# Optimization experiments

Measured on AMD Instinct MI355X. Metric: run time of the kernel, lower is better.

## Reference

```python
import jax, jax.numpy as jnp
import numpy as np

B, C, L, D = 8, 16, 512, 256  # batch, channels (attended axis), seq len, d_model


def setup_inputs() -> dict:
    key = jax.random.key(0)
    ks = jax.random.split(key, 9)
    d = D
    x = jax.random.normal(ks[0], (B, C, L, D), dtype=jnp.float32)
    # qkv projection: Linear(d, 3d), xavier_normal weight, zero-ish bias
    Wqkv = jax.random.normal(ks[1], (3 * d, d), dtype=jnp.float32) * (2.0 / (4 * d)) ** 0.5
    bqkv = jnp.zeros((3 * d,), dtype=jnp.float32)
    # additive-attention scorer V: Linear(d, 1)
    Vw = jax.random.normal(ks[2], (1, d), dtype=jnp.float32) * (1.0 / d) ** 0.5
    Vb = jnp.zeros((1,), dtype=jnp.float32)
    bh = jnp.zeros((d,), dtype=jnp.float32)  # nn.Parameter(torch.zeros(d_model))
    ba = jnp.zeros((1,), dtype=jnp.float32)  # nn.Parameter(torch.zeros(1))
    # output projection Linear(d, d)
    Wout = jax.random.normal(ks[3], (d, d), dtype=jnp.float32) * (1.0 / d) ** 0.5
    bout = jnp.zeros((d,), dtype=jnp.float32)
    return {"x": x, "Wqkv": Wqkv, "bqkv": bqkv, "Vw": Vw, "Vb": Vb,
            "bh": bh, "ba": ba, "Wout": Wout, "bout": bout}


def reference(x, Wqkv, bqkv, Vw, Vb, bh, ba, Wout, bout):
    b, c, l, d = x.shape
    # (b, c, l, d) -> (b*l, c, d): attention over the channel axis c per position
    xf = jnp.transpose(x, (0, 2, 1, 3)).reshape(b * l, c, d)
    qkv = xf @ Wqkv.T + bqkv                       # (B, c, 3d)
    q, k, v = jnp.split(qkv, 3, axis=-1)           # each (B, c, d)
    # additive (Bahdanau) score: V(tanh(q_i + k_j + bh)) + ba
    h = jnp.tanh(q[:, :, None, :] + k[:, None, :, :] + bh)  # (B, c, c, d)
    score = jnp.einsum('bqkd,d->bqk', h, Vw[0]) + Vb[0] + ba[0]  # (B, c, c)
    A = jax.nn.softmax(score, axis=-1)             # stable softmax (matches exp(s-max)/sum)
    # torch einsum 'b c c, b c d -> b c d': repeated index -> DIAGONAL of A scales v
    z = jnp.einsum('bcc,bcd->bcd', A, v)           # (B, c, d)
    z = z.reshape(b, l, c, d).transpose(0, 2, 1, 3)  # (b, c, l, d)
    return z @ Wout.T + bout
```

## Files before the change

kernel.cpp:

```cpp
#include <hip/hip_runtime.h>


typedef __attribute__((ext_vector_type(8))) short bf16x8;
typedef __attribute__((ext_vector_type(4))) float f32x4;
typedef __attribute__((ext_vector_type(8))) _Float16 h16x8;
typedef __attribute__((ext_vector_type(4))) _Float16 h16x4;
typedef const __attribute__((address_space(1))) void* gp1_t;
typedef __attribute__((address_space(3))) void* lp3_t;

__device__ __forceinline__ unsigned short f2bf(float f) {
  union { float f; unsigned int u; } v; v.f = f;
  return (unsigned short)((v.u + 0x7FFFu + ((v.u >> 16) & 1u)) >> 16);
}

__device__ __forceinline__ unsigned int cvt_pk_bf16(float a, float b) {
  unsigned int r;
  asm("v_cvt_pk_bf16_f32 %0, %1, %2" : "=v"(r) : "v"(a), "v"(b));
  return r;
}

__global__ __launch_bounds__(256) void ca_prep_kernel(
    const float* __restrict__ Wqkv, const float* __restrict__ Wout,
    const float* __restrict__ bqkv, const float* __restrict__ bh,
    unsigned short* __restrict__ Wqb_t, unsigned short* __restrict__ Wcb_t,
    float* __restrict__ bcomb, float* __restrict__ bsc) {
  const int blk = blockIdx.x;
  if (blk < 64) {
    const int t = blk * 256 + threadIdx.x;
    const int k8 = t >> 9, n = t & 511;
    const float* src = Wqkv + (size_t)n * 256 + k8 * 8;
    const float4 v0 = *(const float4*)src;
    const float4 v1 = *(const float4*)(src + 4);
    bf16x8 o;
    o[0] = (short)f2bf(v0.x); o[1] = (short)f2bf(v0.y);
    o[2] = (short)f2bf(v0.z); o[3] = (short)f2bf(v0.w);
    o[4] = (short)f2bf(v1.x); o[5] = (short)f2bf(v1.y);
    o[6] = (short)f2bf(v1.z); o[7] = (short)f2bf(v1.w);
    *(bf16x8*)(Wqb_t + (size_t)t * 8) = o;
    return;
  }
  const int dp = blk - 64;
  const int e = threadIdx.x;
  if (dp < 2) {
    const int n = dp * 256 + e;
    const float b = bqkv[n] + (n < 256 ? bh[n] : 0.f);
    bsc[n] = b * 1.4426950408889634f;
  }
  const float* wrow = Wout + (size_t)dp * 256;
  float acc = 0.f;
  for (int f = 0; f < 256; ++f)
    acc = fmaf(wrow[f], Wqkv[(size_t)(512 + f) * 256 + e], acc);
  Wcb_t[((size_t)(e >> 3) * 256 + dp) * 8 + (e & 7)] = f2bf(acc);
  if (e == 0) {
    float b = 0.f;
    for (int f = 0; f < 256; ++f) b = fmaf(wrow[f], bqkv[512 + f], b);
    bcomb[dp] = b;
  }
}

__global__ __launch_bounds__(512, 6) void ca_fused(
    const float* __restrict__ x,
    const unsigned short* __restrict__ Wqb_t,
    const unsigned short* __restrict__ Wcb_t,
    const float* __restrict__ bsc,
    const float* __restrict__ Vw,
    const float* __restrict__ bcomb, const float* __restrict__ bout,
    float* __restrict__ out) {
  __shared__ __align__(16) unsigned short xs[32 * 264];
  __shared__ __align__(16) unsigned short BsEs[16640];
  __shared__ __align__(16) float vw_s[256];
  __shared__ float af_s[32];
  unsigned short* const Bs = BsEs;
  _Float16* const Es = (_Float16*)BsEs;

  const int tid = threadIdx.x;
  const int lane = tid & 63, wave = tid >> 6;
  const int quad = lane >> 4, l15 = lane & 15;
  const int rt0 = blockIdx.x * 32;

  if (tid < 256) vw_s[tid] = -2.f * Vw[tid];

#pragma unroll
  for (int i = 0; i < 4; ++i) {
    const int sb = wave * 256 + i * 64;
    const unsigned short* g = Wqb_t + (size_t)(sb + lane) * 8;
    __builtin_amdgcn_global_load_lds((gp1_t)g, (lp3_t)(Bs + sb * 8), 16, 0, 0);
  }

  {
    const int rl = tid >> 4, c0 = (tid & 15) * 16;
    const int r = rt0 + rl;
    const int b = r >> 13, l = (r >> 4) & 511, c = r & 15;
    const float* src = x + ((size_t)(b * 16 + c) * 512 + l) * 256 + c0;
    unsigned short* dst = xs + rl * 264 + c0;
#pragma unroll
    for (int j = 0; j < 2; ++j) {
      const float4 v0 = *(const float4*)(src + j * 8);
      const float4 v1 = *(const float4*)(src + j * 8 + 4);
      uint4 o;
      o.x = cvt_pk_bf16(v0.x, v0.y);
      o.y = cvt_pk_bf16(v0.z, v0.w);
      o.z = cvt_pk_bf16(v1.x, v1.y);
      o.w = cvt_pk_bf16(v1.z, v1.w);
      *(uint4*)(dst + j * 8) = o;
    }
  }
  __syncthreads();

  f32x4 acc[2][4] = {};
  for (int k0c = 0; k0c < 8; ++k0c) {
    bf16x8 af[2], bfr[4];
#pragma unroll
    for (int mi = 0; mi < 2; ++mi)
      af[mi] = *(const bf16x8*)&xs[(mi * 16 + l15) * 264 + k0c * 32 + quad * 8];
#pragma unroll
    for (int ni = 0; ni < 4; ++ni)
      bfr[ni] = *(const bf16x8*)&Bs[(quad * 512 + wave * 64 + ni * 16 + l15) * 8];
    __syncthreads();
    if (k0c < 7) {
#pragma unroll
      for (int i = 0; i < 4; ++i) {
        const int sb = wave * 256 + i * 64;
        const unsigned short* g =
            Wqb_t + ((size_t)(k0c + 1) * 2048 + sb + lane) * 8;
        __builtin_amdgcn_global_load_lds((gp1_t)g, (lp3_t)(Bs + sb * 8), 16, 0, 0);
      }
    }
#pragma unroll
    for (int mi = 0; mi < 2; ++mi)
#pragma unroll
      for (int ni = 0; ni < 4; ++ni)
        acc[mi][ni] = __builtin_amdgcn_mfma_f32_16x16x32_bf16(
            bfr[ni], af[mi], acc[mi][ni], 0, 0, 0);
    __syncthreads();
  }

#pragma unroll
  for (int mi = 0; mi < 2; ++mi) {
    const int rl = mi * 16 + l15;
#pragma unroll
    for (int ni = 0; ni < 4; ++ni) {
      const int n = wave * 64 + ni * 16 + quad * 4;
      const float4 bs = *(const float4*)(bsc + n);
      const float SC2 = 1.4426950408889634f;
      h16x4 st;
      st[0] = (_Float16)__builtin_amdgcn_exp2f(
          fminf(7.5f, fmaxf(-7.5f, fmaf(acc[mi][ni][0], SC2, bs.x))));
      st[1] = (_Float16)__builtin_amdgcn_exp2f(
          fminf(7.5f, fmaxf(-7.5f, fmaf(acc[mi][ni][1], SC2, bs.y))));
      st[2] = (_Float16)__builtin_amdgcn_exp2f(
          fminf(7.5f, fmaxf(-7.5f, fmaf(acc[mi][ni][2], SC2, bs.z))));
      st[3] = (_Float16)__builtin_amdgcn_exp2f(
          fminf(7.5f, fmaxf(-7.5f, fmaf(acc[mi][ni][3], SC2, bs.w))));
      *(h16x4*)&Es[rl * 520 + n] = st;
    }
  }
  __syncthreads();

  {
    const int p = tid >> 8, qc = (tid >> 4) & 15, kc = tid & 15;
    const _Float16* eqp = Es + (p * 16 + qc) * 520;
    const _Float16* ekp = Es + (p * 16 + kc) * 520 + 256;
    const h16x8 one8 = {(_Float16)1.f, (_Float16)1.f, (_Float16)1.f,
                        (_Float16)1.f, (_Float16)1.f, (_Float16)1.f,
                        (_Float16)1.f, (_Float16)1.f};
    f32x4 a4 = {};
#pragma unroll 4
    for (int d = 0; d < 256; d += 8) {
      const h16x8 eq = *(const h16x8*)(eqp + d);
      const h16x8 ek = *(const h16x8*)(ekp + d);
      const h16x8 pr = eq * ek;
      const h16x8 xm = pr * pr + one8;
      const f32x4 wv0 = *(const f32x4*)(vw_s + d);
      const f32x4 wv1 = *(const f32x4*)(vw_s + d + 4);
      f32x4 sg0, sg1;
      sg0.x = __builtin_amdgcn_rcpf((float)xm[0]);
      sg0.y = __builtin_amdgcn_rcpf((float)xm[1]);
      sg0.z = __builtin_amdgcn_rcpf((float)xm[2]);
      sg0.w = __builtin_amdgcn_rcpf((float)xm[3]);
      sg1.x = __builtin_amdgcn_rcpf((float)xm[4]);
      sg1.y = __builtin_amdgcn_rcpf((float)xm[5]);
      sg1.z = __builtin_amdgcn_rcpf((float)xm[6]);
      sg1.w = __builtin_amdgcn_rcpf((float)xm[7]);
      a4 += wv0 * sg0 + wv1 * sg1;
    }
    float s = (a4[0] + a4[1]) + (a4[2] + a4[3]);
    float m = s;
    for (int off = 8; off; off >>= 1) m = fmaxf(m, __shfl_xor(m, off, 16));
    const float e = __builtin_amdgcn_exp2f((s - m) * 1.4426950408889634f);
    float sum = e;
    for (int off = 8; off; off >>= 1) sum += __shfl_xor(sum, off, 16);
    if (kc == qc) af_s[p * 16 + qc] = e / sum;
  }
  __syncthreads();

#pragma unroll
  for (int i = 0; i < 2; ++i) {
    const int sb = wave * 128 + i * 64;
    const unsigned short* g = Wcb_t + (size_t)(sb + lane) * 8;
    __builtin_amdgcn_global_load_lds((gp1_t)g, (lp3_t)(Bs + sb * 8), 16, 0, 0);
  }
  __syncthreads();

  f32x4 acc2[2][2] = {};
  for (int k0c = 0; k0c < 8; ++k0c) {
    bf16x8 af[2], bfr[2];
#pragma unroll
    for (int mi = 0; mi < 2; ++mi)
      af[mi] = *(const bf16x8*)&xs[(mi * 16 + l15) * 264 + k0c * 32 + quad * 8];
#pragma unroll
    for (int ni = 0; ni < 2; ++ni)
      bfr[ni] = *(const bf16x8*)&Bs[(quad * 256 + wave * 32 + ni * 16 + l15) * 8];
    __syncthreads();
    if (k0c < 7) {
#pragma unroll
      for (int i = 0; i < 2; ++i) {
        const int sb = wave * 128 + i * 64;
        const unsigned short* g =
            Wcb_t + ((size_t)(k0c + 1) * 1024 + sb + lane) * 8;
        __builtin_amdgcn_global_load_lds((gp1_t)g, (lp3_t)(Bs + sb * 8), 16, 0, 0);
      }
    }
#pragma unroll
    for (int mi = 0; mi < 2; ++mi)
#pragma unroll
      for (int ni = 0; ni < 2; ++ni)
        acc2[mi][ni] = __builtin_amdgcn_mfma_f32_16x16x32_bf16(
            bfr[ni], af[mi], acc2[mi][ni], 0, 0, 0);
    __syncthreads();
  }

#pragma unroll
  for (int mi = 0; mi < 2; ++mi) {
    const int rl = mi * 16 + l15;
    const int r = rt0 + rl;
    const int c = r & 15, p = r >> 4;
    const int l = p & 511, b = p >> 9;
    const float av = af_s[rl];
    float* orow = out + ((size_t)(b * 16 + c) * 512 + l) * 256;
#pragma unroll
    for (int ni = 0; ni < 2; ++ni) {
      const int n = wave * 32 + ni * 16 + quad * 4;
      const float4 bc = *(const float4*)(bcomb + n);
      const float4 bo = *(const float4*)(bout + n);
      float4 o;
      o.x = fmaf(av, acc2[mi][ni][0] + bc.x, bo.x);
      o.y = fmaf(av, acc2[mi][ni][1] + bc.y, bo.y);
      o.z = fmaf(av, acc2[mi][ni][2] + bc.z, bo.z);
      o.w = fmaf(av, acc2[mi][ni][3] + bc.w, bo.w);
      *(float4*)(orow + n) = o;
    }
  }
}

extern "C" void kernel_launch(void* const* d_in, const int* in_sizes, int n_in,
                              void* d_out, int out_size, void* d_ws, size_t ws_size,
                              hipStream_t stream) {
  (void)in_sizes; (void)n_in; (void)out_size; (void)ws_size;
  const float* x    = (const float*)d_in[0];
  const float* Wqkv = (const float*)d_in[1];
  const float* bqkv = (const float*)d_in[2];
  const float* Vw   = (const float*)d_in[3];
  const float* bh   = (const float*)d_in[5];
  const float* Wout = (const float*)d_in[7];
  const float* bout = (const float*)d_in[8];
  float* out = (float*)d_out;

  float* bcomb = (float*)d_ws;
  float* bsc = bcomb + 256;
  unsigned short* Wqb_t = (unsigned short*)(bsc + 512);
  unsigned short* Wcb_t = Wqb_t + (size_t)512 * 256;

  ca_prep_kernel<<<dim3(320), dim3(256), 0, stream>>>(
      Wqkv, Wout, bqkv, bh, Wqb_t, Wcb_t, bcomb, bsc);
  ca_fused<<<dim3(2048), dim3(512), 0, stream>>>(
      x, Wqb_t, Wcb_t, bsc, Vw, bcomb, bout, out);
}
```

Baseline: 200.7 us.

## Double-buffer weight tiles with depth-2 async LDS prefetch and explicit waitcnt barriers

Both GEMM phases now split the weight stream into smaller chunks and double-buffer them in LDS. Each chunk is prefetched two iterations ahead via global_load_lds, and the code waits with explicit vmcnt and raw s_barrier instead of two __syncthreads per step. The x tile load is also issued before the first weight prefetch so the global latencies overlap. The aim is to hide weight-load latency behind the MFMAs and cut barrier overhead, at the cost of more loop iterations and fragile hand-managed wait counts.

```diff
diff --git a/kernel.cpp b/kernel.cpp
--- a/kernel.cpp
+++ b/kernel.cpp
@@ -7,6 +7,9 @@
 typedef __attribute__((ext_vector_type(4))) _Float16 h16x4;
 typedef const __attribute__((address_space(1))) void* gp1_t;
 typedef __attribute__((address_space(3))) void* lp3_t;
+
+#define SBAR() __builtin_amdgcn_s_barrier()
+#define SCHED_FENCE() __builtin_amdgcn_sched_barrier(0)
 
 __device__ __forceinline__ unsigned short f2bf(float f) {
   union { float f; unsigned int u; } v; v.f = f;
@@ -70,7 +73,6 @@
   __shared__ __align__(16) unsigned short BsEs[16640];
   __shared__ __align__(16) float vw_s[256];
   __shared__ float af_s[32];
-  unsigned short* const Bs = BsEs;
   _Float16* const Es = (_Float16*)BsEs;
 
   const int tid = threadIdx.x;
@@ -80,79 +82,97 @@
 
   if (tid < 256) vw_s[tid] = -2.f * Vw[tid];
 
-#pragma unroll
-  for (int i = 0; i < 4; ++i) {
-    const int sb = wave * 256 + i * 64;
-    const unsigned short* g = Wqb_t + (size_t)(sb + lane) * 8;
-    __builtin_amdgcn_global_load_lds((gp1_t)g, (lp3_t)(Bs + sb * 8), 16, 0, 0);
-  }
-
+  const int rl = tid >> 4, cc0 = (tid & 15) * 16;
+  const float* xsrc;
   {
-    const int rl = tid >> 4, c0 = (tid & 15) * 16;
     const int r = rt0 + rl;
     const int b = r >> 13, l = (r >> 4) & 511, c = r & 15;
-    const float* src = x + ((size_t)(b * 16 + c) * 512 + l) * 256 + c0;
-    unsigned short* dst = xs + rl * 264 + c0;
-#pragma unroll
-    for (int j = 0; j < 2; ++j) {
-      const float4 v0 = *(const float4*)(src + j * 8);
-      const float4 v1 = *(const float4*)(src + j * 8 + 4);
-      uint4 o;
-      o.x = cvt_pk_bf16(v0.x, v0.y);
-      o.y = cvt_pk_bf16(v0.z, v0.w);
-      o.z = cvt_pk_bf16(v1.x, v1.y);
-      o.w = cvt_pk_bf16(v1.z, v1.w);
-      *(uint4*)(dst + j * 8) = o;
-    }
-  }
-  __syncthreads();
+    xsrc = x + ((size_t)(b * 16 + c) * 512 + l) * 256 + cc0;
+  }
+  const float4 va = *(const float4*)(xsrc);
+  const float4 vb = *(const float4*)(xsrc + 4);
+  const float4 vc = *(const float4*)(xsrc + 8);
+  const float4 vd = *(const float4*)(xsrc + 12);
+
+#pragma unroll
+  for (int c = 0; c < 2; ++c) {
+    unsigned short* buf = BsEs + (c & 1) * 8192;
+#pragma unroll
+    for (int i = 0; i < 2; ++i) {
+      const int s = wave * 128 + i * 64 + lane;
+      const unsigned short* g =
+          Wqb_t + (size_t)(((c & 7) * 4 + (s >> 8)) * 512 + (c >> 3) * 256 +
+                           (s & 255)) * 8;
+      __builtin_amdgcn_global_load_lds((gp1_t)g, (lp3_t)(buf + s * 8), 16, 0, 0);
+    }
+  }
+
+  {
+    unsigned short* dst = xs + rl * 264 + cc0;
+    uint4 o0, o1;
+    o0.x = cvt_pk_bf16(va.x, va.y); o0.y = cvt_pk_bf16(va.z, va.w);
+    o0.z = cvt_pk_bf16(vb.x, vb.y); o0.w = cvt_pk_bf16(vb.z, vb.w);
+    o1.x = cvt_pk_bf16(vc.x, vc.y); o1.y = cvt_pk_bf16(vc.z, vc.w);
+    o1.z = cvt_pk_bf16(vd.x, vd.y); o1.w = cvt_pk_bf16(vd.z, vd.w);
+    *(uint4*)(dst) = o0;
+    *(uint4*)(dst + 8) = o1;
+  }
+  asm volatile("s_waitcnt lgkmcnt(0)" ::: "memory");
+  SCHED_FENCE(); SBAR(); SCHED_FENCE();
 
   f32x4 acc[2][4] = {};
-  for (int k0c = 0; k0c < 8; ++k0c) {
-    bf16x8 af[2], bfr[4];
+#pragma unroll
+  for (int c = 0; c < 16; ++c) {
+    if (c < 15) { asm volatile("s_waitcnt vmcnt(2)" ::: "memory"); }
+    else        { asm volatile("s_waitcnt vmcnt(0)" ::: "memory"); }
+    SCHED_FENCE(); SBAR(); SCHED_FENCE();
+    unsigned short* buf = BsEs + (c & 1) * 8192;
+    const int kc = c & 7, p2 = (c >> 3) * 2;
+    bf16x8 af[2], bfr[2];
 #pragma unroll
     for (int mi = 0; mi < 2; ++mi)
-      af[mi] = *(const bf16x8*)&xs[(mi * 16 + l15) * 264 + k0c * 32 + quad * 8];
-#pragma unroll
-    for (int ni = 0; ni < 4; ++ni)
-      bfr[ni] = *(const bf16x8*)&Bs[(quad * 512 + wave * 64 + ni * 16 + l15) * 8];
-    __syncthreads();
-    if (k0c < 7) {
-#pragma unroll
-      for (int i = 0; i < 4; ++i) {
-        const int sb = wave * 256 + i * 64;
+      af[mi] = *(const bf16x8*)&xs[(mi * 16 + l15) * 264 + kc * 32 + quad * 8];
+#pragma unroll
+    for (int ni = 0; ni < 2; ++ni)
+      bfr[ni] = *(const bf16x8*)&buf[(quad * 256 + wave * 32 + ni * 16 + l15) * 8];
+#pragma unroll
+    for (int mi = 0; mi < 2; ++mi)
+#pragma unroll
+      for (int ni = 0; ni < 2; ++ni)
+        acc[mi][p2 + ni] = __builtin_amdgcn_mfma_f32_16x16x32_bf16(
+            bfr[ni], af[mi], acc[mi][p2 + ni], 0, 0, 0);
+    SCHED_FENCE(); SBAR();
+    if (c + 2 < 16) {
+      const int cn = c + 2;
+#pragma unroll
+      for (int i = 0; i < 2; ++i) {
+        const int s = wave * 128 + i * 64 + lane;
         const unsigned short* g =
-            Wqb_t + ((size_t)(k0c + 1) * 2048 + sb + lane) * 8;
-        __builtin_amdgcn_global_load_lds((gp1_t)g, (lp3_t)(Bs + sb * 8), 16, 0, 0);
+            Wqb_t + (size_t)(((cn & 7) * 4 + (s >> 8)) * 512 +
+                             (cn >> 3) * 256 + (s & 255)) * 8;
+        __builtin_amdgcn_global_load_lds((gp1_t)g, (lp3_t)(buf + s * 8), 16, 0, 0);
       }
     }
-#pragma unroll
-    for (int mi = 0; mi < 2; ++mi)
-#pragma unroll
-      for (int ni = 0; ni < 4; ++ni)
-        acc[mi][ni] = __builtin_amdgcn_mfma_f32_16x16x32_bf16(
-            bfr[ni], af[mi], acc[mi][ni], 0, 0, 0);
-    __syncthreads();
   }
 
 #pragma unroll
   for (int mi = 0; mi < 2; ++mi) {
-    const int rl = mi * 16 + l15;
-#pragma unroll
-    for (int ni = 0; ni < 4; ++ni) {
-      const int n = wave * 64 + ni * 16 + quad * 4;
+    const int rr = mi * 16 + l15;
+#pragma unroll
+    for (int j = 0; j < 4; ++j) {
+      const int n = (j >> 1) * 256 + wave * 32 + (j & 1) * 16 + quad * 4;
       const float4 bs = *(const float4*)(bsc + n);
       const float SC2 = 1.4426950408889634f;
       h16x4 st;
       st[0] = (_Float16)__builtin_amdgcn_exp2f(
-          fminf(7.5f, fmaxf(-7.5f, fmaf(acc[mi][ni][0], SC2, bs.x))));
+          fminf(7.5f, fmaxf(-7.5f, fmaf(acc[mi][j][0], SC2, bs.x))));
       st[1] = (_Float16)__builtin_amdgcn_exp2f(
-          fminf(7.5f, fmaxf(-7.5f, fmaf(acc[mi][ni][1], SC2, bs.y))));
+          fminf(7.5f, fmaxf(-7.5f, fmaf(acc[mi][j][1], SC2, bs.y))));
       st[2] = (_Float16)__builtin_amdgcn_exp2f(
-          fminf(7.5f, fmaxf(-7.5f, fmaf(acc[mi][ni][2], SC2, bs.z))));
+          fminf(7.5f, fmaxf(-7.5f, fmaf(acc[mi][j][2], SC2, bs.z))));
       st[3] = (_Float16)__builtin_amdgcn_exp2f(
-          fminf(7.5f, fmaxf(-7.5f, fmaf(acc[mi][ni][3], SC2, bs.w))));
-      *(h16x4*)&Es[rl * 520 + n] = st;
+          fminf(7.5f, fmaxf(-7.5f, fmaf(acc[mi][j][3], SC2, bs.w))));
+      *(h16x4*)&Es[rr * 520 + n] = st;
     }
   }
   __syncthreads();
@@ -195,48 +215,54 @@
   __syncthreads();
 
 #pragma unroll
-  for (int i = 0; i < 2; ++i) {
-    const int sb = wave * 128 + i * 64;
-    const unsigned short* g = Wcb_t + (size_t)(sb + lane) * 8;
-    __builtin_amdgcn_global_load_lds((gp1_t)g, (lp3_t)(Bs + sb * 8), 16, 0, 0);
-  }
-  __syncthreads();
-
+  for (int c = 0; c < 2; ++c) {
+    unsigned short* buf = BsEs + (c & 1) * 8192;
+#pragma unroll
+    for (int i = 0; i < 2; ++i) {
+      const int s = wave * 128 + i * 64 + lane;
+      const unsigned short* g = Wcb_t + (size_t)(c * 1024 + s) * 8;
+      __builtin_amdgcn_global_load_lds((gp1_t)g, (lp3_t)(buf + s * 8), 16, 0, 0);
+    }
+  }
   f32x4 acc2[2][2] = {};
-  for (int k0c = 0; k0c < 8; ++k0c) {
+#pragma unroll
+  for (int c = 0; c < 8; ++c) {
+    if (c < 7) { asm volatile("s_waitcnt vmcnt(2)" ::: "memory"); }
+    else       { asm volatile("s_waitcnt vmcnt(0)" ::: "memory"); }
+    SCHED_FENCE(); SBAR(); SCHED_FENCE();
+    unsigned short* buf = BsEs + (c & 1) * 8192;
     bf16x8 af[2], bfr[2];
 #pragma unroll
     for (int mi = 0; mi < 2; ++mi)
-      af[mi] = *(const bf16x8*)&xs[(mi * 16 + l15) * 264 + k0c * 32 + quad * 8];
+      af[mi] = *(const bf16x8*)&xs[(mi * 16 + l15) * 264 + c * 32 + quad * 8];
 #pragma unroll
     for (int ni = 0; ni < 2; ++ni)
-      bfr[ni] = *(const bf16x8*)&Bs[(quad * 256 + wave * 32 + ni * 16 + l15) * 8];
-    __syncthreads();
-    if (k0c < 7) {
-#pragma unroll
-      for (int i = 0; i < 2; ++i) {
-        const int sb = wave * 128 + i * 64;
-        const unsigned short* g =
-            Wcb_t + ((size_t)(k0c + 1) * 1024 + sb + lane) * 8;
-        __builtin_amdgcn_global_load_lds((gp1_t)g, (lp3_t)(Bs + sb * 8), 16, 0, 0);
-      }
-    }
+      bfr[ni] = *(const bf16x8*)&buf[(quad * 256 + wave * 32 + ni * 16 + l15) * 8];
 #pragma unroll
     for (int mi = 0; mi < 2; ++mi)
 #pragma unroll
       for (int ni = 0; ni < 2; ++ni)
         acc2[mi][ni] = __builtin_amdgcn_mfma_f32_16x16x32_bf16(
             bfr[ni], af[mi], acc2[mi][ni], 0, 0, 0);
-    __syncthreads();
+    SCHED_FENCE(); SBAR();
+    if (c + 2 < 8) {
+      const int cn = c + 2;
+#pragma unroll
+      for (int i = 0; i < 2; ++i) {
+        const int s = wave * 128 + i * 64 + lane;
+        const unsigned short* g = Wcb_t + (size_t)(cn * 1024 + s) * 8;
+        __builtin_amdgcn_global_load_lds((gp1_t)g, (lp3_t)(buf + s * 8), 16, 0, 0);
+      }
+    }
   }
 
 #pragma unroll
   for (int mi = 0; mi < 2; ++mi) {
-    const int rl = mi * 16 + l15;
-    const int r = rt0 + rl;
+    const int rr = mi * 16 + l15;
+    const int r = rt0 + rr;
     const int c = r & 15, p = r >> 4;
     const int l = p & 511, b = p >> 9;
-    const float av = af_s[rl];
+    const float av = af_s[rr];
     float* orow = out + ((size_t)(b * 16 + c) * 512 + l) * 256;
 #pragma unroll
     for (int ni = 0; ni < 2; ++ni) {
```

New measurement: 198.5 us. About the same (-1.1%).
